# Performance work log

Measured on AMD Instinct MI355X. Metric: run time of the kernel, lower is better.

The kernel has to match this reference:

```python
import jax, jax.numpy as jnp
import numpy as np

SEQ, BATCH, IN, RES = 1024, 64, 512, 2048

def setup_inputs() -> dict:
    key = jax.random.key(0)
    k1, k2, k3, k4 = jax.random.split(key, 4)
    x = jax.random.normal(k1, (SEQ, BATCH, IN), dtype=jnp.float32)
    # ESN reservoir weights: untrained random matrices (spectral-radius style scaling)
    W_in = jax.random.normal(k2, (RES, IN), dtype=jnp.float32) * 0.1
    W_hh = jax.random.normal(k3, (RES, RES), dtype=jnp.float32) * (0.9 / jnp.sqrt(RES))
    b = jax.random.normal(k4, (RES,), dtype=jnp.float32) * 0.1
    return {"x": x, "W_in": W_in, "W_hh": W_hh, "b": b}

def reference(x, W_in, W_hh, b):
    # ESNBase.forward -> _forward_type_2 with num_layers=1, unidirectional.
    # h_t = tanh(x_t @ W_in^T + h_{t-1} @ W_hh^T + b)
    batch = x.shape[1]
    h0 = jnp.zeros((batch, W_hh.shape[0]), dtype=x.dtype)
    # Precompute input projection for all steps (parallel GEMM), scan the recurrence.
    xin = jnp.einsum('sbi,ri->sbr', x, W_in) + b  # (seq, batch, res)
    def step(h, u):
        h_new = jnp.tanh(u + h @ W_hh.T)
        return h_new, h_new
    h_n, states = jax.lax.scan(step, h0, xin)
    # output: (seq, batch, num_directions*hidden); h_n: (num_layers*num_directions, batch, hidden)
    return states, h_n[None, :, :]
```

## Files before the change

kernel.cpp:

```cpp
#include <hip/hip_runtime.h>
#include <hip/hip_bf16.h>


#define SEQ 1024
#define NB  64
#define INF 512
#define RES 2048

typedef float    f32x4 __attribute__((ext_vector_type(4)));
typedef _Float16 f16x8 __attribute__((ext_vector_type(8)));

__device__ __forceinline__ float fast_tanh(float x) {
  const float e = __expf(2.0f * x);
  return 1.0f - 2.0f * __builtin_amdgcn_rcpf(1.0f + e);
}

__global__ __launch_bounds__(256) void xin_gemm(
    const float* __restrict__ X, const float* __restrict__ Win,
    const float* __restrict__ bias, float* __restrict__ U)
{
  __shared__ _Float16 lA[2][128][40];
  __shared__ _Float16 lB[2][128][40];

  const int tid  = threadIdx.x;
  const int lane = tid & 63;
  const int wv   = tid >> 6;
  const int wr   = wv >> 1;
  const int wc   = wv & 1;
  const int m0   = (blockIdx.x >> 4) * 128;
  const int n0   = (blockIdx.x & 15) * 128;

  const int srow = tid >> 1;
  const int sk   = (tid & 1) * 16;

  const int fr = lane & 15;
  const int fk = (lane >> 4) * 8;

  f32x4 acc[4][4] = {};
  float ra[16], rb[16];

  const float* xa_base = X   + (size_t)(m0 + srow) * INF + sk;
  const float* xb_base = Win + (size_t)(n0 + srow) * INF + sk;

#define LOADK(kt) do {                                                     \
    const float* pa = xa_base + (kt) * 32;                                 \
    const float* pb = xb_base + (kt) * 32;                                 \
    *(f32x4*)&ra[0]  = *(const f32x4*)(pa + 0);                            \
    *(f32x4*)&ra[4]  = *(const f32x4*)(pa + 4);                            \
    *(f32x4*)&ra[8]  = *(const f32x4*)(pa + 8);                            \
    *(f32x4*)&ra[12] = *(const f32x4*)(pa + 12);                           \
    *(f32x4*)&rb[0]  = *(const f32x4*)(pb + 0);                            \
    *(f32x4*)&rb[4]  = *(const f32x4*)(pb + 4);                            \
    *(f32x4*)&rb[8]  = *(const f32x4*)(pb + 8);                            \
    *(f32x4*)&rb[12] = *(const f32x4*)(pb + 12);                           \
  } while (0)

#define STOREK(buf) do {                                                   \
    f16x8 h0, h1;                                                          \
    _Pragma("unroll") for (int j = 0; j < 8; ++j) h0[j] = (_Float16)ra[j]; \
    _Pragma("unroll") for (int j = 0; j < 8; ++j) h1[j] = (_Float16)ra[8+j];\
    *(f16x8*)&lA[buf][srow][sk]     = h0;                                  \
    *(f16x8*)&lA[buf][srow][sk + 8] = h1;                                  \
    _Pragma("unroll") for (int j = 0; j < 8; ++j) h0[j] = (_Float16)rb[j]; \
    _Pragma("unroll") for (int j = 0; j < 8; ++j) h1[j] = (_Float16)rb[8+j];\
    *(f16x8*)&lB[buf][srow][sk]     = h0;                                  \
    *(f16x8*)&lB[buf][srow][sk + 8] = h1;                                  \
  } while (0)

#define COMPUTE(buf) do {                                                  \
    f16x8 af[4], bf[4];                                                    \
    _Pragma("unroll") for (int mt = 0; mt < 4; ++mt)                       \
      af[mt] = *(const f16x8*)&lA[buf][wr*64 + mt*16 + fr][fk];            \
    _Pragma("unroll") for (int nt = 0; nt < 4; ++nt)                       \
      bf[nt] = *(const f16x8*)&lB[buf][wc*64 + nt*16 + fr][fk];            \
    _Pragma("unroll") for (int mt = 0; mt < 4; ++mt)                       \
      _Pragma("unroll") for (int nt = 0; nt < 4; ++nt)                     \
        acc[mt][nt] = __builtin_amdgcn_mfma_f32_16x16x32_f16(              \
            af[mt], bf[nt], acc[mt][nt], 0, 0, 0);                         \
  } while (0)

  LOADK(0);
  STOREK(0);
  __syncthreads();

#pragma unroll 1
  for (int kt = 0; kt < 16; ++kt) {
    const int buf = kt & 1;
    if (kt < 15) LOADK(kt + 1);
    COMPUTE(buf);
    if (kt < 15) STOREK(buf ^ 1);
    __syncthreads();
  }

#pragma unroll
  for (int mt = 0; mt < 4; ++mt) {
    const int row = m0 + wr*64 + mt*16 + (lane >> 4) * 4;
#pragma unroll
    for (int nt = 0; nt < 4; ++nt) {
      const int col = n0 + wc*64 + nt*16 + fr;
      const float bv = bias[col];
#pragma unroll
      for (int i = 0; i < 4; ++i)
        U[(size_t)(row + i) * RES + col] = acc[mt][nt][i] + bv;
    }
  }
#undef LOADK
#undef STOREK
#undef COMPUTE
}

#define WPAD 2056

__global__ __launch_bounds__(512, 1) void esn_recur(
    const float* __restrict__ Whh, float* __restrict__ states,
    float* __restrict__ hn, _Float16* __restrict__ hbuf,
    unsigned* __restrict__ flags)
{
  __shared__ _Float16 Wl[32 * WPAD];
  __shared__ f32x4    red0[8][64];
  __shared__ f32x4    red1[8][64];

  const int tid  = threadIdx.x;
  const int lane = tid & 63;
  const int wv   = tid >> 6;
  const int q    = wv;

  const int bid = blockIdx.x;
  const int xg  = bid & 7;
  const int bg  = xg >> 1;
  const int cg  = ((xg & 1) << 5) | (bid >> 3);
  const int b0  = bg * 16;
  const int c0  = cg * 32;

  {
    const int row = tid >> 4;
    const int ch  = tid & 15;
    const float* src = Whh + (size_t)(c0 + row) * RES + ch * 128;
    _Float16* dst = Wl + row * WPAD + ch * 128;
#pragma unroll 4
    for (int i = 0; i < 128; i += 4) {
      f32x4 v = *(const f32x4*)(src + i);
      dst[i + 0] = (_Float16)v.x;
      dst[i + 1] = (_Float16)v.y;
      dst[i + 2] = (_Float16)v.z;
      dst[i + 3] = (_Float16)v.w;
    }
  }
  __syncthreads();

  const int fr = lane & 15;
  const int fk = (lane >> 4) * 8;

  const _Float16* const wp0 = Wl + fr * WPAD + q * 256 + fk;
  const _Float16* const wp1 = wp0 + 16 * WPAD;

  _Float16* const hbuf0 = hbuf;
  _Float16* const hbuf1 = hbuf + (size_t)NB * RES;
  unsigned* const fb = flags + bg * (128 * 32);

  for (int s = 0; s < SEQ; ++s) {
    f32x4 a0 = {0.f, 0.f, 0.f, 0.f}, a1 = {0.f, 0.f, 0.f, 0.f};

    float u[4];
    if (wv < 2) {
      const float* up = states + (size_t)s * NB * RES;
      const int col = c0 + wv * 16 + fr;
#pragma unroll
      for (int i = 0; i < 4; ++i) {
        const int b = b0 + (lane >> 4) * 4 + i;
        u[i] = up[(size_t)b * RES + col];
      }
    }

    if (s > 0) {
      const _Float16* hp = ((s & 1) ? hbuf0 : hbuf1)
                         + (size_t)(b0 + fr) * RES + q * 256 + fk;
#pragma unroll
      for (int ks = 0; ks < 8; ++ks) {
        union { unsigned long long w[2]; f16x8 v; } au;
        au.w[0] = __hip_atomic_load((const unsigned long long*)(hp + ks * 32),
                                    __ATOMIC_RELAXED, __HIP_MEMORY_SCOPE_AGENT);
        au.w[1] = __hip_atomic_load((const unsigned long long*)(hp + ks * 32 + 4),
                                    __ATOMIC_RELAXED, __HIP_MEMORY_SCOPE_AGENT);
        const f16x8 w0 = *(const f16x8*)(wp0 + ks * 32);
        const f16x8 w1 = *(const f16x8*)(wp1 + ks * 32);
        a0 = __builtin_amdgcn_mfma_f32_16x16x32_f16(au.v, w0, a0, 0, 0, 0);
        a1 = __builtin_amdgcn_mfma_f32_16x16x32_f16(au.v, w1, a1, 0, 0, 0);
      }
    }

    red0[q][lane] = a0;
    red1[q][lane] = a1;
    __syncthreads();

    if (wv < 2) {
      const f32x4 (* __restrict__ rp)[64] = wv ? red1 : red0;
      f32x4 acc = rp[0][lane];
#pragma unroll
      for (int j = 1; j < 8; ++j) acc += rp[j][lane];

      float* up = states + (size_t)s * NB * RES;
      unsigned short* hc16 = (unsigned short*)((s & 1) ? hbuf1 : hbuf0);
      const int col = c0 + wv * 16 + fr;
#pragma unroll
      for (int i = 0; i < 4; ++i) {
        const int b = b0 + (lane >> 4) * 4 + i;
        const size_t off = (size_t)b * RES + col;
        const float v = fast_tanh(u[i] + acc[i]);
        up[off] = v;
        const _Float16 vh = (_Float16)v;
        __hip_atomic_store(&hc16[off], __builtin_bit_cast(unsigned short, vh),
                           __ATOMIC_RELAXED, __HIP_MEMORY_SCOPE_AGENT);
        if (s == SEQ - 1) hn[off] = v;
      }
      asm volatile("s_waitcnt vmcnt(0)" ::: "memory");
      if (lane == 0)
        __hip_atomic_store(fb + (wv * 64 + cg) * 32, (unsigned)(s + 1),
                           __ATOMIC_RELAXED, __HIP_MEMORY_SCOPE_AGENT);
    } else if (wv == 2) {
      const unsigned tgt = (unsigned)(s + 1);
      for (;;) {
        const unsigned va = __hip_atomic_load(fb + lane * 32,
                              __ATOMIC_RELAXED, __HIP_MEMORY_SCOPE_AGENT);
        const unsigned vb = __hip_atomic_load(fb + (64 + lane) * 32,
                              __ATOMIC_RELAXED, __HIP_MEMORY_SCOPE_AGENT);
        if (__all((va >= tgt) & (vb >= tgt))) break;
      }
    }
    __syncthreads();
  }
}

extern "C" void kernel_launch(void* const* d_in, const int* in_sizes, int n_in,
                              void* d_out, int out_size, void* d_ws, size_t ws_size,
                              hipStream_t stream) {
  const float* x    = (const float*)d_in[0];
  const float* W_in = (const float*)d_in[1];
  const float* W_hh = (const float*)d_in[2];
  const float* bias = (const float*)d_in[3];

  float* states = (float*)d_out;
  float* hn     = states + (size_t)SEQ * NB * RES;

  _Float16* hbuf  = (_Float16*)d_ws;
  unsigned* flags = (unsigned*)((char*)d_ws + (size_t)2 * NB * RES * sizeof(_Float16));

  hipMemsetAsync(flags, 0, (size_t)4 * 128 * 32 * sizeof(unsigned), stream);

  xin_gemm<<<dim3(512 * 16), dim3(256), 0, stream>>>(x, W_in, bias, states);
  esn_recur<<<dim3(256), dim3(512), 0, stream>>>(W_hh, states, hn, hbuf, flags);
}
```

Measured before the change: 7.109 ms.

## Replace per-step flag barrier with NaN-sentinel ring buffer and register-resident weights

The recurrent kernel now keeps its slice of W_hh in registers as fp16 fragments instead of LDS. The hidden state moves to a 16-slot ring buffer poisoned with NaN sentinels, so consumers spin on the data itself instead of waiting on a per-step flag barrier. The global flag barrier now runs only every 8 steps, and at that point producers re-poison the next 8 slots. This removes the per-step grid-wide synchronisation latency, at the cost of higher register pressure, extra sentinel stores, a full-ring memset, and correctness that depends on relaxed-atomic visibility ordering and on tanh never producing a NaN or Inf.

```diff
diff --git a/kernel.cpp b/kernel.cpp
--- a/kernel.cpp
+++ b/kernel.cpp
@@ -2,10 +2,11 @@
 #include <hip/hip_bf16.h>
 
 
-#define SEQ 1024
-#define NB  64
-#define INF 512
-#define RES 2048
+#define SEQ  1024
+#define NB   64
+#define INF  512
+#define RES  2048
+#define RING 16
 
 typedef float    f32x4 __attribute__((ext_vector_type(4)));
 typedef _Float16 f16x8 __attribute__((ext_vector_type(8)));
@@ -109,16 +110,13 @@
 #undef COMPUTE
 }
 
-#define WPAD 2056
-
 __global__ __launch_bounds__(512, 1) void esn_recur(
     const float* __restrict__ Whh, float* __restrict__ states,
-    float* __restrict__ hn, _Float16* __restrict__ hbuf,
+    float* __restrict__ hn, _Float16* __restrict__ ring,
     unsigned* __restrict__ flags)
 {
-  __shared__ _Float16 Wl[32 * WPAD];
-  __shared__ f32x4    red0[8][64];
-  __shared__ f32x4    red1[8][64];
+  __shared__ f32x4 red0[8][64];
+  __shared__ f32x4 red1[8][64];
 
   const int tid  = threadIdx.x;
   const int lane = tid & 63;
@@ -132,30 +130,25 @@
   const int b0  = bg * 16;
   const int c0  = cg * 32;
 
-  {
-    const int row = tid >> 4;
-    const int ch  = tid & 15;
-    const float* src = Whh + (size_t)(c0 + row) * RES + ch * 128;
-    _Float16* dst = Wl + row * WPAD + ch * 128;
-#pragma unroll 4
-    for (int i = 0; i < 128; i += 4) {
-      f32x4 v = *(const f32x4*)(src + i);
-      dst[i + 0] = (_Float16)v.x;
-      dst[i + 1] = (_Float16)v.y;
-      dst[i + 2] = (_Float16)v.z;
-      dst[i + 3] = (_Float16)v.w;
-    }
-  }
-  __syncthreads();
-
   const int fr = lane & 15;
   const int fk = (lane >> 4) * 8;
 
-  const _Float16* const wp0 = Wl + fr * WPAD + q * 256 + fk;
-  const _Float16* const wp1 = wp0 + 16 * WPAD;
-
-  _Float16* const hbuf0 = hbuf;
-  _Float16* const hbuf1 = hbuf + (size_t)NB * RES;
+  f16x8 wf[2][8];
+#pragma unroll
+  for (int ct = 0; ct < 2; ++ct) {
+#pragma unroll
+    for (int ks = 0; ks < 8; ++ks) {
+      const float* wsrc = Whh + (size_t)(c0 + ct*16 + fr) * RES
+                        + q*256 + ks*32 + fk;
+      const f32x4 w0 = *(const f32x4*)(wsrc);
+      const f32x4 w1 = *(const f32x4*)(wsrc + 4);
+      f16x8 f;
+#pragma unroll
+      for (int j = 0; j < 4; ++j) { f[j] = (_Float16)w0[j]; f[4+j] = (_Float16)w1[j]; }
+      wf[ct][ks] = f;
+    }
+  }
+
   unsigned* const fb = flags + bg * (128 * 32);
 
   for (int s = 0; s < SEQ; ++s) {
@@ -166,26 +159,40 @@
       const float* up = states + (size_t)s * NB * RES;
       const int col = c0 + wv * 16 + fr;
 #pragma unroll
-      for (int i = 0; i < 4; ++i) {
-        const int b = b0 + (lane >> 4) * 4 + i;
-        u[i] = up[(size_t)b * RES + col];
-      }
+      for (int i = 0; i < 4; ++i)
+        u[i] = up[(size_t)(b0 + (lane >> 4) * 4 + i) * RES + col];
     }
 
     if (s > 0) {
-      const _Float16* hp = ((s & 1) ? hbuf0 : hbuf1)
+      const _Float16* hp = ring + (size_t)((s - 1) & (RING - 1)) * NB * RES
                          + (size_t)(b0 + fr) * RES + q * 256 + fk;
+      f16x8 hv[8];
+      for (;;) {
+#pragma unroll
+        for (int ks = 0; ks < 8; ++ks) {
+          union { unsigned long long w[2]; f16x8 v; } au;
+          au.w[0] = __hip_atomic_load((const unsigned long long*)(hp + ks*32),
+                                      __ATOMIC_RELAXED, __HIP_MEMORY_SCOPE_AGENT);
+          au.w[1] = __hip_atomic_load((const unsigned long long*)(hp + ks*32 + 4),
+                                      __ATOMIC_RELAXED, __HIP_MEMORY_SCOPE_AGENT);
+          hv[ks] = au.v;
+        }
+        f16x8 t0 = hv[0] + hv[1], t1 = hv[2] + hv[3];
+        f16x8 t2 = hv[4] + hv[5], t3 = hv[6] + hv[7];
+        f16x8 ss = (t0 + t1) + (t2 + t3);
+        union { f16x8 v; unsigned w[4]; } su; su.v = ss;
+        unsigned bad = 0;
+#pragma unroll
+        for (int j = 0; j < 4; ++j) {
+          bad |= ((su.w[j] & 0x7C00u) == 0x7C00u);
+          bad |= (((su.w[j] >> 16) & 0x7C00u) == 0x7C00u);
+        }
+        if (!__any(bad)) break;
+      }
 #pragma unroll
       for (int ks = 0; ks < 8; ++ks) {
-        union { unsigned long long w[2]; f16x8 v; } au;
-        au.w[0] = __hip_atomic_load((const unsigned long long*)(hp + ks * 32),
-                                    __ATOMIC_RELAXED, __HIP_MEMORY_SCOPE_AGENT);
-        au.w[1] = __hip_atomic_load((const unsigned long long*)(hp + ks * 32 + 4),
-                                    __ATOMIC_RELAXED, __HIP_MEMORY_SCOPE_AGENT);
-        const f16x8 w0 = *(const f16x8*)(wp0 + ks * 32);
-        const f16x8 w1 = *(const f16x8*)(wp1 + ks * 32);
-        a0 = __builtin_amdgcn_mfma_f32_16x16x32_f16(au.v, w0, a0, 0, 0, 0);
-        a1 = __builtin_amdgcn_mfma_f32_16x16x32_f16(au.v, w1, a1, 0, 0, 0);
+        a0 = __builtin_amdgcn_mfma_f32_16x16x32_f16(hv[ks], wf[0][ks], a0, 0, 0, 0);
+        a1 = __builtin_amdgcn_mfma_f32_16x16x32_f16(hv[ks], wf[1][ks], a1, 0, 0, 0);
       }
     }
 
@@ -193,6 +200,8 @@
     red1[q][lane] = a1;
     __syncthreads();
 
+    const bool barrier_step = ((s & 7) == 7) && (s != SEQ - 1);
+
     if (wv < 2) {
       const f32x4 (* __restrict__ rp)[64] = wv ? red1 : red0;
       f32x4 acc = rp[0][lane];
@@ -200,7 +209,8 @@
       for (int j = 1; j < 8; ++j) acc += rp[j][lane];
 
       float* up = states + (size_t)s * NB * RES;
-      unsigned short* hc16 = (unsigned short*)((s & 1) ? hbuf1 : hbuf0);
+      unsigned short* hc16 = (unsigned short*)(ring
+                           + (size_t)(s & (RING - 1)) * NB * RES);
       const int col = c0 + wv * 16 + fr;
 #pragma unroll
       for (int i = 0; i < 4; ++i) {
@@ -214,11 +224,26 @@
         if (s == SEQ - 1) hn[off] = v;
       }
       asm volatile("s_waitcnt vmcnt(0)" ::: "memory");
-      if (lane == 0)
-        __hip_atomic_store(fb + (wv * 64 + cg) * 32, (unsigned)(s + 1),
-                           __ATOMIC_RELAXED, __HIP_MEMORY_SCOPE_AGENT);
-    } else if (wv == 2) {
-      const unsigned tgt = (unsigned)(s + 1);
+
+      if (barrier_step) {
+#pragma unroll
+        for (int d = 1; d <= 8; ++d) {
+          unsigned short* pz = (unsigned short*)(ring
+                             + (size_t)((s + d) & (RING - 1)) * NB * RES);
+#pragma unroll
+          for (int i = 0; i < 4; ++i) {
+            const size_t off = (size_t)(b0 + (lane >> 4) * 4 + i) * RES + col;
+            __hip_atomic_store(&pz[off], (unsigned short)0x7F7Fu,
+                               __ATOMIC_RELAXED, __HIP_MEMORY_SCOPE_AGENT);
+          }
+        }
+        asm volatile("s_waitcnt vmcnt(0)" ::: "memory");
+        if (lane == 0)
+          __hip_atomic_store(fb + (wv * 64 + cg) * 32, (unsigned)((s >> 3) + 1),
+                             __ATOMIC_RELAXED, __HIP_MEMORY_SCOPE_AGENT);
+      }
+    } else if (wv == 2 && barrier_step) {
+      const unsigned tgt = (unsigned)((s >> 3) + 1);
       for (;;) {
         const unsigned va = __hip_atomic_load(fb + lane * 32,
                               __ATOMIC_RELAXED, __HIP_MEMORY_SCOPE_AGENT);
@@ -242,11 +267,13 @@
   float* states = (float*)d_out;
   float* hn     = states + (size_t)SEQ * NB * RES;
 
-  _Float16* hbuf  = (_Float16*)d_ws;
-  unsigned* flags = (unsigned*)((char*)d_ws + (size_t)2 * NB * RES * sizeof(_Float16));
-
+  _Float16* ring  = (_Float16*)d_ws;
+  unsigned* flags = (unsigned*)((char*)d_ws
+                  + (size_t)RING * NB * RES * sizeof(_Float16));
+
+  hipMemsetAsync(ring, 0x7F, (size_t)RING * NB * RES * sizeof(_Float16), stream);
   hipMemsetAsync(flags, 0, (size_t)4 * 128 * 32 * sizeof(unsigned), stream);
 
   xin_gemm<<<dim3(512 * 16), dim3(256), 0, stream>>>(x, W_in, bias, states);
-  esn_recur<<<dim3(256), dim3(512), 0, stream>>>(W_hh, states, hn, hbuf, flags);
-}
+  esn_recur<<<dim3(256), dim3(512), 0, stream>>>(W_hh, states, hn, ring, flags);
+}
```

Result: faster. 6.679 ms (-6.1%).
